# Kernel optimization log

Hardware: AMD Instinct MI355X
Metric: run time of the kernel (lower is better)

The kernel has to match this reference:

```python
import jax, jax.numpy as jnp
import numpy as np

# Stack of L SSA transformer blocks (SMVDR conv_trans stages with sr_ratio=2)
L, B, N, C = 4, 64, 196, 768          # layers, batch(=16 samples x 4 views), tokens, dim
CN = 960                               # c_new = int(C * 1.25)
HID = 3072                             # mlp hidden = 4*C
NH = 12                                # heads
HD, HDK = C // NH, CN // NH            # v head dim 64, q/k head dim 80
SR, HW = 2, 14                         # spatial reduction ratio, sqrt(N)


def _ln(x, g, b, eps):
    m = jnp.mean(x, axis=-1, keepdims=True)
    v = jnp.var(x, axis=-1, keepdims=True)
    return (x - m) * jax.lax.rsqrt(v + eps) * g + b


def setup_inputs() -> dict:
    key = jax.random.key(0)
    ks = jax.random.split(key, 12)
    s = jnp.float32(0.02)

    def rn(k, shape):
        return jax.random.normal(k, shape, jnp.float32) * s

    return {
        "x": jax.random.normal(ks[0], (B, N, C), jnp.float32),
        "q_w": rn(ks[1], (L, C, CN)),                 # q projection (no bias)
        "dw_w": rn(ks[2], (L, C, 1, SR, SR)),         # depthwise reduction conv (OIHW, groups=C)
        "dw_b": jnp.zeros((L, C), jnp.float32),
        "pw_w": rn(ks[3], (L, C, CN)),                # 1x1 conv C -> c_new
        "pw_b": jnp.zeros((L, CN), jnp.float32),
        "lnr_g": jnp.ones((L, CN), jnp.float32),      # norm_act LayerNorm (eps 1e-5)
        "lnr_b": jnp.zeros((L, CN), jnp.float32),
        "k_w": rn(ks[4], (L, CN, CN)),
        "v_w": rn(ks[5], (L, CN, C)),
        "proj_w": rn(ks[6], (L, C, C)),
        "proj_b": jnp.zeros((L, C), jnp.float32),
        "ln1_g": jnp.ones((L, C), jnp.float32),
        "ln1_b": jnp.zeros((L, C), jnp.float32),
        "ln2_g": jnp.ones((L, C), jnp.float32),
        "ln2_b": jnp.zeros((L, C), jnp.float32),
        "fc1_w": rn(ks[7], (L, C, HID)),
        "fc1_b": jnp.zeros((L, HID), jnp.float32),
        "fc2_w": rn(ks[8], (L, HID, C)),
        "fc2_b": jnp.zeros((L, C), jnp.float32),
    }


def reference(x, q_w, dw_w, dw_b, pw_w, pw_b, lnr_g, lnr_b, k_w, v_w,
              proj_w, proj_b, ln1_g, ln1_b, ln2_g, ln2_b,
              fc1_w, fc1_b, fc2_w, fc2_b):
    scale = 1.0 / jnp.sqrt(jnp.float32(HD) * 1.25)   # (head_dim * c_ratio) ** -0.5
    for l in range(L):
        # --- SSA attention branch ---
        y = _ln(x, ln1_g[l], ln1_b[l], 1e-6)
        img = y.transpose(0, 2, 1).reshape(B, C, HW, HW)
        # strided depthwise conv reduction (kernel=stride=sr_ratio, groups=C)
        r = jax.lax.conv_general_dilated(
            img, dw_w[l], window_strides=(SR, SR), padding='VALID',
            feature_group_count=C,
            dimension_numbers=('NCHW', 'OIHW', 'NCHW'))
        r = r + dw_b[l][None, :, None, None]
        r = jnp.einsum('bchw,cd->bhwd', r, pw_w[l]) + pw_b[l]   # 1x1 conv -> (B,7,7,CN)
        r = r.reshape(B, -1, CN)                                 # (B, M=49, CN)
        r = jax.nn.gelu(_ln(r, lnr_g[l], lnr_b[l], 1e-5), approximate=False)
        q = (y @ q_w[l]).reshape(B, N, NH, HDK).transpose(0, 2, 1, 3)   # (B,H,N,80)
        k = (r @ k_w[l]).reshape(B, -1, NH, HDK).transpose(0, 2, 1, 3)  # (B,H,M,80)
        v = (r @ v_w[l]).reshape(B, -1, NH, HD).transpose(0, 2, 1, 3)   # (B,H,M,64)
        attn = jax.nn.softmax(jnp.einsum('bhnd,bhmd->bhnm', q, k) * scale, axis=-1)
        o = jnp.einsum('bhnm,bhmd->bnhd', attn, v).reshape(B, N, C)
        x = x + o @ proj_w[l] + proj_b[l]
        # --- MLP branch ---
        z = _ln(x, ln2_g[l], ln2_b[l], 1e-6)
        h = jax.nn.gelu(z @ fc1_w[l] + fc1_b[l], approximate=False)
        x = x + h @ fc2_w[l] + fc2_b[l]
    return x
```

## Files before the change

### kernel.cpp

```cpp
#include <hip/hip_runtime.h>
#include <hip/hip_bf16.h>
#include <math.h>

#define L_LAYERS 4
#define BSZ 64
#define NTOK 196
#define CDIM 768
#define CNDIM 960
#define HIDDIM 3072
#define NHEAD 12
#define HD 64
#define HDK 80
#define MRED 49
#define ROWS (BSZ*NTOK)
#define RROWS (BSZ*MRED)
#define KVN 1728

typedef __bf16 bf16x8 __attribute__((ext_vector_type(8)));
typedef float f32x4 __attribute__((ext_vector_type(4)));
typedef unsigned short u16x4 __attribute__((ext_vector_type(4)));

static __device__ inline float bf2f(unsigned short u) {
    unsigned int x = ((unsigned int)u) << 16;
    return __builtin_bit_cast(float, x);
}
static __device__ inline unsigned short f2bf(float f) {
    return __builtin_bit_cast(unsigned short, __float2bfloat16(f));
}
static __device__ inline unsigned int pack2bf(float lo, float hi) {
    return (unsigned int)f2bf(lo) | ((unsigned int)f2bf(hi) << 16);
}
static __device__ inline float gelu_f(float x) {
    float t = x * (1.5957691216f + 0.0713548162f * x * x);
    return x * __builtin_amdgcn_rcpf(1.0f + __expf(-t));
}

#define GLLDS16(gsrc, ldst)                                                        \
    __builtin_amdgcn_global_load_lds(                                              \
        (const __attribute__((address_space(1))) unsigned int*)(const void*)(gsrc),\
        (__attribute__((address_space(3))) unsigned int*)(void*)(ldst), 16, 0, 0)

__global__ void transpose_bf16_kernel(const float* __restrict__ src,
                                      unsigned short* __restrict__ dst,
                                      int K, int N, size_t srcLS, size_t dstLS) {
    __shared__ float tile[32][33];
    const float* s = src + (size_t)blockIdx.z * srcLS;
    unsigned short* d = dst + (size_t)blockIdx.z * dstLS;
    int k0 = blockIdx.y * 32, n0 = blockIdx.x * 32;
#pragma unroll
    for (int i = 0; i < 4; i++) {
        int k = k0 + threadIdx.y + i * 8, n = n0 + threadIdx.x;
        if (k < K && n < N) tile[threadIdx.y + i * 8][threadIdx.x] = s[(size_t)k * N + n];
    }
    __syncthreads();
#pragma unroll
    for (int i = 0; i < 4; i++) {
        int n = n0 + threadIdx.y + i * 8, k = k0 + threadIdx.x;
        if (n < N && k < K) d[(size_t)n * K + k] = f2bf(tile[threadIdx.x][threadIdx.y + i * 8]);
    }
}

__global__ void ln_kernel(const float* __restrict__ x, const float* __restrict__ g,
                          const float* __restrict__ b, unsigned short* __restrict__ y,
                          int M, int C, float eps, int do_gelu) {
    int row = blockIdx.x * 4 + (threadIdx.x >> 6);
    int lane = threadIdx.x & 63;
    if (row >= M) return;
    const float* xr = x + (size_t)row * C;
    float s = 0.f, ss = 0.f;
    for (int c = lane; c < C; c += 64) { float v = xr[c]; s += v; ss += v * v; }
#pragma unroll
    for (int off = 32; off; off >>= 1) { s += __shfl_down(s, off); ss += __shfl_down(ss, off); }
    s = __shfl(s, 0); ss = __shfl(ss, 0);
    float mean = s / (float)C;
    float var = ss / (float)C - mean * mean;
    float rstd = rsqrtf(var + eps);
    unsigned short* yr = y + (size_t)row * C;
    for (int c = lane; c < C; c += 64) {
        float v = (xr[c] - mean) * rstd * g[c] + b[c];
        if (do_gelu) v = gelu_f(v);
        yr[c] = f2bf(v);
    }
}

__global__ void dwconv_kernel(const unsigned short* __restrict__ y,
                              const float* __restrict__ w,
                              const float* __restrict__ bias,
                              unsigned short* __restrict__ r0) {
    int bm = blockIdx.x;
    int b = bm / MRED, m = bm % MRED;
    int i = m / 7, j = m % 7;
    int r00 = b * NTOK + (2 * i) * 14 + 2 * j;
    for (int c = threadIdx.x; c < CDIM; c += 256) {
        float acc = bias[c];
        acc += bf2f(y[(size_t)(r00)      * CDIM + c]) * w[c * 4 + 0];
        acc += bf2f(y[(size_t)(r00 + 1)  * CDIM + c]) * w[c * 4 + 1];
        acc += bf2f(y[(size_t)(r00 + 14) * CDIM + c]) * w[c * 4 + 2];
        acc += bf2f(y[(size_t)(r00 + 15) * CDIM + c]) * w[c * 4 + 3];
        r0[(size_t)bm * CDIM + c] = f2bf(acc);
    }
}

template <int MODE, int BN>
__global__ __launch_bounds__(512, 4) void gemm128_kernel(
    const unsigned short* __restrict__ A,
    const unsigned short* __restrict__ Bt,
    const float* __restrict__ bias,
    float* __restrict__ outF,
    unsigned short* __restrict__ outB,
    int M, int N, int K, int NR, int NC) {
    constexpr int NFR = BN / 64;
    constexpr int SLOT = 8192 + BN * 64;
    extern __shared__ __align__(16) char sb[];

    int id = blockIdx.x;
    int gsize = 8 * NC;
    int g = id / gsize;
    int local = id - g * gsize;
    int rbase = g * 8;
    int Gg = NR - rbase; if (Gg > 8) Gg = 8;
    int col = local / Gg;
    int row = rbase + (local - col * Gg);
    int m0 = row * 128, n0 = col * BN;

    int tid = threadIdx.x;
    int w = tid >> 6, lane = tid & 63, quad = lane >> 4, l16 = lane & 15;
    int wm = w >> 2, wn = w & 3;

    int sr = tid >> 2;
    int qs = ((tid & 3) - ((sr >> 1) & 3)) & 3;
    const unsigned short* aS0 = A  + (size_t)(m0 + sr) * K + qs * 8;
    const unsigned short* bS0 = Bt + (size_t)(n0 + sr) * K + qs * 8;
    const unsigned short* bS1 = Bt + (size_t)(n0 + sr + 128) * K + qs * 8;

    int sq16 = ((quad + (l16 >> 1)) & 3) * 16;
    int aOff = (wm * 64 + l16) * 64 + sq16;
    int bOff = 8192 + (wn * (BN / 4) + l16) * 64 + sq16;

    f32x4 zero4 = {0.f, 0.f, 0.f, 0.f};
    f32x4 acc[4][NFR];
#pragma unroll
    for (int mi = 0; mi < 4; mi++)
#pragma unroll
        for (int ni = 0; ni < NFR; ni++) acc[mi][ni] = zero4;

    int NT = K >> 5;

    {
        GLLDS16(aS0, sb + w * 1024);
        GLLDS16(bS0, sb + 8192 + w * 1024);
        if constexpr (BN == 256) GLLDS16(bS1, sb + 16384 + w * 1024);
    }
    asm volatile("s_waitcnt vmcnt(0)" ::: "memory");
    __builtin_amdgcn_s_barrier();

    for (int t = 0; t < NT; ++t) {
        char* sc = sb + (size_t)(t & 1) * SLOT;
        if (t + 1 < NT) {
            char* sp = sb + (size_t)((t + 1) & 1) * SLOT;
            int koff = (t + 1) * 32;
            GLLDS16(aS0 + koff, sp + w * 1024);
            GLLDS16(bS0 + koff, sp + 8192 + w * 1024);
            if constexpr (BN == 256) GLLDS16(bS1 + koff, sp + 16384 + w * 1024);
        }
        bf16x8 af[4], bfr[NFR];
#pragma unroll
        for (int mi = 0; mi < 4; mi++)
            af[mi] = *(const bf16x8*)(sc + aOff + mi * 1024);
#pragma unroll
        for (int ni = 0; ni < NFR; ni++)
            bfr[ni] = *(const bf16x8*)(sc + bOff + ni * 1024);
        __builtin_amdgcn_s_setprio(1);
#pragma unroll
        for (int mi = 0; mi < 4; mi++)
#pragma unroll
            for (int ni = 0; ni < NFR; ni++)
                acc[mi][ni] = __builtin_amdgcn_mfma_f32_16x16x32_bf16(
                    af[mi], bfr[ni], acc[mi][ni], 0, 0, 0);
        __builtin_amdgcn_s_setprio(0);
        asm volatile("s_waitcnt vmcnt(0)" ::: "memory");
        __builtin_amdgcn_s_barrier();
    }

    __syncthreads();
    float* eld = (float*)(sb + w * (BN == 256 ? 4096 : 2048));
    int colbase = n0 + wn * (BN / 4);
#pragma unroll
    for (int mi = 0; mi < 4; mi++) {
#pragma unroll
        for (int ni = 0; ni < NFR; ni++)
#pragma unroll
            for (int rr = 0; rr < 4; rr++)
                eld[(quad * 4 + rr) * (BN / 4) + ni * 16 + l16] = acc[mi][ni][rr];
        int rowb = m0 + wm * 64 + mi * 16;
        constexpr int NP = (BN == 256) ? 4 : 2;
#pragma unroll
        for (int p = 0; p < NP; p++) {
            int r, c;
            if constexpr (BN == 256) { r = p * 4 + quad;        c = l16 * 4; }
            else                     { r = p * 8 + (lane >> 3); c = (lane & 7) * 4; }
            int gr = rowb + r, gc = colbase + c;
            if (gr < M && gc < N) {
                f32x4 v4 = *(f32x4*)(eld + r * (BN / 4) + c);
                if (MODE == 0) {
                    u16x4 h;
#pragma unroll
                    for (int e = 0; e < 4; e++) h[e] = f2bf(v4[e]);
                    *(u16x4*)(outB + (size_t)gr * N + gc) = h;
                } else {
                    f32x4 b4 = *(const f32x4*)(bias + gc);
                    if (MODE == 1) {
                        *(f32x4*)(outF + (size_t)gr * N + gc) = v4 + b4;
                    } else if (MODE == 2) {
                        f32x4 o4 = *(f32x4*)(outF + (size_t)gr * N + gc);
                        *(f32x4*)(outF + (size_t)gr * N + gc) = o4 + v4 + b4;
                    } else {
                        u16x4 h;
#pragma unroll
                        for (int e = 0; e < 4; e++) h[e] = f2bf(gelu_f(v4[e] + b4[e]));
                        *(u16x4*)(outB + (size_t)gr * N + gc) = h;
                    }
                }
            }
        }
    }
}

__global__ __launch_bounds__(512, 4) void attn_kernel(
    const unsigned short* __restrict__ qb,
    const unsigned short* __restrict__ kv,
    unsigned short* __restrict__ ob) {
    __shared__ __align__(16) unsigned short Ks[64 * 96];
    __shared__ __align__(16) unsigned short V2[64 * 136];
    __shared__ __align__(16) unsigned short Os[8 * 16 * 72];

    int bh = blockIdx.x;
    int b = bh / NHEAD, h = bh % NHEAD;
    int tid = threadIdx.x;

    for (int idx = tid; idx < 49 * 8; idx += 512) {
        int m = idx >> 3, c = idx & 7;
        ((unsigned int*)Ks)[m * 48 + 40 + c] = 0u;
    }
    for (int idx = tid; idx < 49 * 10; idx += 512) {
        int m = idx / 10, c = idx % 10;
        bf16x8 v = *(const bf16x8*)(kv + (size_t)(b * MRED + m) * KVN + h * HDK + c * 8);
        *(bf16x8*)(Ks + m * 96 + c * 8) = v;
    }
    for (int idx = tid; idx < 64 * 128; idx += 512) {
        int d = idx >> 7, c = idx & 127;
        int s = c >> 5, q = (c >> 3) & 3, j = c & 7;
        int kt = s * 32 + ((j >> 2) << 4) + q * 4 + (j & 3);
        unsigned short val = 0;
        if (kt < MRED) val = kv[(size_t)(b * MRED + kt) * KVN + 960 + h * HD + d];
        V2[d * 136 + c] = val;
    }
    __syncthreads();

    int wv = tid >> 6, lane = tid & 63, quad = lane >> 4, l16 = lane & 15;
    unsigned short* Ow = Os + wv * 16 * 72;
    const float scale = 0.11180339887498949f;
    f32x4 zero4 = {0.f, 0.f, 0.f, 0.f};

#pragma unroll
    for (int gi = 0; gi < 2; ++gi) {
        int qg = wv + gi * 8;
        if (qg >= 13) break;
        const unsigned short* qrow =
            qb + (size_t)(b * NTOK + qg * 16 + l16) * CNDIM + h * HDK + quad * 8;
        bf16x8 bq0 = *(const bf16x8*)(qrow);
        bf16x8 bq1 = *(const bf16x8*)(qrow + 32);
        bf16x8 bq2 = *(const bf16x8*)(qrow + 64);

        f32x4 sf[4];
#pragma unroll
        for (int kf = 0; kf < 4; kf++) sf[kf] = zero4;
#pragma unroll
        for (int kf = 0; kf < 4; kf++) {
            const unsigned short* kr = Ks + (kf * 16 + l16) * 96 + quad * 8;
            sf[kf] = __builtin_amdgcn_mfma_f32_16x16x32_bf16(
                *(const bf16x8*)(kr), bq0, sf[kf], 0, 0, 0);
            sf[kf] = __builtin_amdgcn_mfma_f32_16x16x32_bf16(
                *(const bf16x8*)(kr + 32), bq1, sf[kf], 0, 0, 0);
            sf[kf] = __builtin_amdgcn_mfma_f32_16x16x32_bf16(
                *(const bf16x8*)(kr + 64), bq2, sf[kf], 0, 0, 0);
        }

        float p[4][4];
        float mx = -1e30f;
#pragma unroll
        for (int kf = 0; kf < 4; kf++)
#pragma unroll
            for (int r = 0; r < 4; r++) {
                float v = sf[kf][r] * scale;
                if (kf == 3) {
                    v = (r == 0 && quad == 0) ? v : -1e30f;
                }
                p[kf][r] = v;
                mx = fmaxf(mx, v);
            }
        mx = fmaxf(mx, __shfl_xor(mx, 16));
        mx = fmaxf(mx, __shfl_xor(mx, 32));
        float sum = 0.f;
#pragma unroll
        for (int kf = 0; kf < 4; kf++)
#pragma unroll
            for (int r = 0; r < 4; r++) {
                float e = __expf(p[kf][r] - mx);
                p[kf][r] = e;
                sum += e;
            }
        sum += __shfl_xor(sum, 16);
        sum += __shfl_xor(sum, 32);
        float inv = 1.0f / sum;
#pragma unroll
        for (int kf = 0; kf < 4; kf++)
#pragma unroll
            for (int r = 0; r < 4; r++) p[kf][r] *= inv;

        unsigned int W[4][2];
#pragma unroll
        for (int kf = 0; kf < 4; kf++) {
            W[kf][0] = pack2bf(p[kf][0], p[kf][1]);
            W[kf][1] = pack2bf(p[kf][2], p[kf][3]);
        }

        f32x4 oacc[4];
#pragma unroll
        for (int df = 0; df < 4; df++) oacc[df] = zero4;
#pragma unroll
        for (int s = 0; s < 2; s++) {
            union { unsigned int u[4]; bf16x8 v; } bb;
            bb.u[0] = W[2 * s][0];
            bb.u[1] = W[2 * s][1];
            bb.u[2] = W[2 * s + 1][0];
            bb.u[3] = W[2 * s + 1][1];
#pragma unroll
            for (int df = 0; df < 4; df++) {
                const unsigned short* vr = V2 + (df * 16 + l16) * 136 + s * 32 + quad * 8;
                oacc[df] = __builtin_amdgcn_mfma_f32_16x16x32_bf16(
                    *(const bf16x8*)(vr), bb.v, oacc[df], 0, 0, 0);
            }
        }

#pragma unroll
        for (int df = 0; df < 4; df++) {
#pragma unroll
            for (int wp = 0; wp < 2; wp++) {
                unsigned int pk = pack2bf(oacc[df][2 * wp], oacc[df][2 * wp + 1]);
                *(unsigned int*)(Ow + l16 * 72 + df * 16 + quad * 4 + 2 * wp) = pk;
            }
        }
        int q = lane >> 2, cch = lane & 3;
        int grow = qg * 16 + q;
        if (grow < NTOK) {
            unsigned short* dst = ob + (size_t)(b * NTOK + grow) * CDIM + h * HD + cch * 8;
            bf16x8 v0 = *(const bf16x8*)(Ow + q * 72 + cch * 8);
            bf16x8 v1 = *(const bf16x8*)(Ow + q * 72 + cch * 8 + 32);
            *(bf16x8*)(dst) = v0;
            *(bf16x8*)(dst + 32) = v1;
        }
    }
}


extern "C" void kernel_launch(void* const* d_in, const int* in_sizes, int n_in,
                              void* d_out, int out_size, void* d_ws, size_t ws_size,
                              hipStream_t stream) {
    (void)in_sizes; (void)n_in; (void)out_size; (void)ws_size;
    const float* x_in   = (const float*)d_in[0];
    const float* q_w    = (const float*)d_in[1];
    const float* dw_w   = (const float*)d_in[2];
    const float* dw_b   = (const float*)d_in[3];
    const float* pw_w   = (const float*)d_in[4];
    const float* pw_b   = (const float*)d_in[5];
    const float* lnr_g  = (const float*)d_in[6];
    const float* lnr_b  = (const float*)d_in[7];
    const float* k_w    = (const float*)d_in[8];
    const float* v_w    = (const float*)d_in[9];
    const float* proj_w = (const float*)d_in[10];
    const float* proj_b = (const float*)d_in[11];
    const float* ln1_g  = (const float*)d_in[12];
    const float* ln1_b  = (const float*)d_in[13];
    const float* ln2_g  = (const float*)d_in[14];
    const float* ln2_b  = (const float*)d_in[15];
    const float* fc1_w  = (const float*)d_in[16];
    const float* fc1_b  = (const float*)d_in[17];
    const float* fc2_w  = (const float*)d_in[18];
    const float* fc2_b  = (const float*)d_in[19];
    float* xout = (float*)d_out;
    char* ws = (char*)d_ws;

    const size_t PL = 8601600;
    const size_t offQ = 0, offPW = 786432, offKV = 1572864,
                 offPJ = 3293184, offF1 = 3883008, offF2 = 6242304;
    unsigned short* W = (unsigned short*)ws;
    char* act = ws + PL * 2 * L_LAYERS;
    unsigned short* y_bf = (unsigned short*)act;
    char* blk = act + (size_t)ROWS * CDIM * 2;
    unsigned short* q_bf  = (unsigned short*)(blk);
    unsigned short* r0_bf = (unsigned short*)(blk + 24084480);
    float*          pw_f  = (float*)        (blk + 29196288);
    unsigned short* r_bf  = (unsigned short*)(blk + 41238528);
    unsigned short* kv_bf = (unsigned short*)(blk + 47628288);
    unsigned short* o_bf  = (unsigned short*)(blk + 58466304);
    unsigned short* h_bf  = (unsigned short*)(blk);
    unsigned short* z_bf  = y_bf;

    hipMemcpyAsync(xout, x_in, (size_t)ROWS * CDIM * sizeof(float),
                   hipMemcpyDeviceToDevice, stream);

    dim3 tb(32, 8);
    transpose_bf16_kernel<<<dim3(CNDIM / 32, CDIM / 32, L_LAYERS), tb, 0, stream>>>(
        q_w, W + offQ, CDIM, CNDIM, (size_t)CDIM * CNDIM, PL);
    transpose_bf16_kernel<<<dim3(CNDIM / 32, CDIM / 32, L_LAYERS), tb, 0, stream>>>(
        pw_w, W + offPW, CDIM, CNDIM, (size_t)CDIM * CNDIM, PL);
    transpose_bf16_kernel<<<dim3(CNDIM / 32, CNDIM / 32, L_LAYERS), tb, 0, stream>>>(
        k_w, W + offKV, CNDIM, CNDIM, (size_t)CNDIM * CNDIM, PL);
    transpose_bf16_kernel<<<dim3(CDIM / 32, CNDIM / 32, L_LAYERS), tb, 0, stream>>>(
        v_w, W + offKV + (size_t)CNDIM * CNDIM, CNDIM, CDIM, (size_t)CNDIM * CDIM, PL);
    transpose_bf16_kernel<<<dim3(CDIM / 32, CDIM / 32, L_LAYERS), tb, 0, stream>>>(
        proj_w, W + offPJ, CDIM, CDIM, (size_t)CDIM * CDIM, PL);
    transpose_bf16_kernel<<<dim3(HIDDIM / 32, CDIM / 32, L_LAYERS), tb, 0, stream>>>(
        fc1_w, W + offF1, CDIM, HIDDIM, (size_t)CDIM * HIDDIM, PL);
    transpose_bf16_kernel<<<dim3(CDIM / 32, HIDDIM / 32, L_LAYERS), tb, 0, stream>>>(
        fc2_w, W + offF2, HIDDIM, CDIM, (size_t)HIDDIM * CDIM, PL);

    for (int l = 0; l < L_LAYERS; l++) {
        const unsigned short* wl = W + (size_t)l * PL;
        ln_kernel<<<ROWS / 4, 256, 0, stream>>>(xout, ln1_g + l * CDIM, ln1_b + l * CDIM,
                                                y_bf, ROWS, CDIM, 1e-6f, 0);
        gemm128_kernel<0, 256><<<98 * 4, 512, 49152, stream>>>(
            y_bf, wl + offQ, nullptr, nullptr, q_bf, ROWS, CNDIM, CDIM, 98, 4);
        dwconv_kernel<<<RROWS, 256, 0, stream>>>(y_bf, dw_w + (size_t)l * CDIM * 4,
                                                 dw_b + l * CDIM, r0_bf);
        gemm128_kernel<1, 128><<<25 * 8, 512, 32768, stream>>>(
            r0_bf, wl + offPW, pw_b + l * CNDIM, pw_f, nullptr, RROWS, CNDIM, CDIM, 25, 8);
        ln_kernel<<<RROWS / 4, 256, 0, stream>>>(pw_f, lnr_g + l * CNDIM, lnr_b + l * CNDIM,
                                                 r_bf, RROWS, CNDIM, 1e-5f, 1);
        gemm128_kernel<0, 128><<<25 * 14, 512, 32768, stream>>>(
            r_bf, wl + offKV, nullptr, nullptr, kv_bf, RROWS, KVN, CNDIM, 25, 14);
        attn_kernel<<<BSZ * NHEAD, 512, 0, stream>>>(q_bf, kv_bf, o_bf);
        gemm128_kernel<2, 256><<<98 * 3, 512, 49152, stream>>>(
            o_bf, wl + offPJ, proj_b + l * CDIM, xout, nullptr, ROWS, CDIM, CDIM, 98, 3);
        ln_kernel<<<ROWS / 4, 256, 0, stream>>>(xout, ln2_g + l * CDIM, ln2_b + l * CDIM,
                                                z_bf, ROWS, CDIM, 1e-6f, 0);
        gemm128_kernel<3, 256><<<98 * 12, 512, 49152, stream>>>(
            z_bf, wl + offF1, fc1_b + l * HIDDIM, nullptr, h_bf, ROWS, HIDDIM, CDIM, 98, 12);
        gemm128_kernel<2, 256><<<98 * 3, 512, 49152, stream>>>(
            h_bf, wl + offF2, fc2_b + l * CDIM, xout, nullptr, ROWS, CDIM, HIDDIM, 98, 3);
    }
}
```

Before: 1.597 ms.

## Triple-buffer GEMM K-loop and split-K residual GEMMs with atomic accumulation

The GEMM main loop moves from a double-buffered LDS pipeline to three slots, keeping two tiles of global-to-LDS loads in flight with partial vmcnt waits. The residual-add GEMMs (proj with split 2, fc2 with split 4) gain a split-K mode: more workgroups each handle a slice of K and add into the output with float atomics, bias added only by the first slice. This targets load latency and the low workgroup count of the N=768 GEMMs (294 blocks). In exchange it needs more LDS per block, which can reduce occupancy, and adds atomic traffic with a nondeterministic summation order.

Result: slower. 4.098 ms (+156.7%).

```diff
diff --git a/kernel.cpp b/kernel.cpp
--- a/kernel.cpp
+++ b/kernel.cpp
@@ -101,7 +101,7 @@
     }
 }
 
-template <int MODE, int BN>
+template <int MODE, int BN, int SK>
 __global__ __launch_bounds__(512, 4) void gemm128_kernel(
     const unsigned short* __restrict__ A,
     const unsigned short* __restrict__ Bt,
@@ -111,9 +111,13 @@
     int M, int N, int K, int NR, int NC) {
     constexpr int NFR = BN / 64;
     constexpr int SLOT = 8192 + BN * 64;
+    constexpr int LPS = (BN == 256) ? 3 : 2;
     extern __shared__ __align__(16) char sb[];
 
     int id = blockIdx.x;
+    int per = NR * NC;
+    int ks = 0;
+    if constexpr (SK > 1) { ks = id / per; id -= ks * per; }
     int gsize = 8 * NC;
     int g = id / gsize;
     int local = id - g * gsize;
@@ -122,6 +126,8 @@
     int col = local / Gg;
     int row = rbase + (local - col * Gg);
     int m0 = row * 128, n0 = col * BN;
+    int KS = K / SK;
+    int k0 = ks * KS;
 
     int tid = threadIdx.x;
     int w = tid >> 6, lane = tid & 63, quad = lane >> 4, l16 = lane & 15;
@@ -129,9 +135,9 @@
 
     int sr = tid >> 2;
     int qs = ((tid & 3) - ((sr >> 1) & 3)) & 3;
-    const unsigned short* aS0 = A  + (size_t)(m0 + sr) * K + qs * 8;
-    const unsigned short* bS0 = Bt + (size_t)(n0 + sr) * K + qs * 8;
-    const unsigned short* bS1 = Bt + (size_t)(n0 + sr + 128) * K + qs * 8;
+    const unsigned short* aS0 = A  + (size_t)(m0 + sr) * K + k0 + qs * 8;
+    const unsigned short* bS0 = Bt + (size_t)(n0 + sr) * K + k0 + qs * 8;
+    const unsigned short* bS1 = Bt + (size_t)(n0 + sr + 128) * K + k0 + qs * 8;
 
     int sq16 = ((quad + (l16 >> 1)) & 3) * 16;
     int aOff = (wm * 64 + l16) * 64 + sq16;
@@ -144,24 +150,32 @@
 #pragma unroll
         for (int ni = 0; ni < NFR; ni++) acc[mi][ni] = zero4;
 
-    int NT = K >> 5;
-
-    {
-        GLLDS16(aS0, sb + w * 1024);
-        GLLDS16(bS0, sb + 8192 + w * 1024);
-        if constexpr (BN == 256) GLLDS16(bS1, sb + 16384 + w * 1024);
-    }
-    asm volatile("s_waitcnt vmcnt(0)" ::: "memory");
+    int NT = KS >> 5;
+
+#define STAGE3(slotptr, tt)                                                \
+    do {                                                                   \
+        int koff_ = (tt) * 32;                                             \
+        GLLDS16(aS0 + koff_, (slotptr) + w * 1024);                        \
+        GLLDS16(bS0 + koff_, (slotptr) + 8192 + w * 1024);                 \
+        if constexpr (BN == 256) GLLDS16(bS1 + koff_, (slotptr) + 16384 + w * 1024); \
+    } while (0)
+
+    STAGE3(sb, 0);
+    if (NT > 1) {
+        STAGE3(sb + SLOT, 1);
+        if constexpr (BN == 256) asm volatile("s_waitcnt vmcnt(3)" ::: "memory");
+        else                     asm volatile("s_waitcnt vmcnt(2)" ::: "memory");
+    } else {
+        asm volatile("s_waitcnt vmcnt(0)" ::: "memory");
+    }
     __builtin_amdgcn_s_barrier();
 
+    int sC = 0;
     for (int t = 0; t < NT; ++t) {
-        char* sc = sb + (size_t)(t & 1) * SLOT;
-        if (t + 1 < NT) {
-            char* sp = sb + (size_t)((t + 1) & 1) * SLOT;
-            int koff = (t + 1) * 32;
-            GLLDS16(aS0 + koff, sp + w * 1024);
-            GLLDS16(bS0 + koff, sp + 8192 + w * 1024);
-            if constexpr (BN == 256) GLLDS16(bS1 + koff, sp + 16384 + w * 1024);
+        char* sc = sb + (size_t)sC * SLOT;
+        if (t + 2 < NT) {
+            int sP = sC + 2; if (sP >= 3) sP -= 3;
+            STAGE3(sb + (size_t)sP * SLOT, t + 2);
         }
         bf16x8 af[4], bfr[NFR];
 #pragma unroll
@@ -178,9 +192,16 @@
                 acc[mi][ni] = __builtin_amdgcn_mfma_f32_16x16x32_bf16(
                     af[mi], bfr[ni], acc[mi][ni], 0, 0, 0);
         __builtin_amdgcn_s_setprio(0);
-        asm volatile("s_waitcnt vmcnt(0)" ::: "memory");
+        if (t + 2 < NT) {
+            if constexpr (BN == 256) asm volatile("s_waitcnt vmcnt(3)" ::: "memory");
+            else                     asm volatile("s_waitcnt vmcnt(2)" ::: "memory");
+        } else {
+            asm volatile("s_waitcnt vmcnt(0)" ::: "memory");
+        }
         __builtin_amdgcn_s_barrier();
-    }
+        sC++; if (sC == 3) sC = 0;
+    }
+#undef STAGE3
 
     __syncthreads();
     float* eld = (float*)(sb + w * (BN == 256 ? 4096 : 2048));
@@ -212,8 +233,18 @@
                     if (MODE == 1) {
                         *(f32x4*)(outF + (size_t)gr * N + gc) = v4 + b4;
                     } else if (MODE == 2) {
-                        f32x4 o4 = *(f32x4*)(outF + (size_t)gr * N + gc);
-                        *(f32x4*)(outF + (size_t)gr * N + gc) = o4 + v4 + b4;
+                        if constexpr (SK == 1) {
+                            f32x4 o4 = *(f32x4*)(outF + (size_t)gr * N + gc);
+                            *(f32x4*)(outF + (size_t)gr * N + gc) = o4 + v4 + b4;
+                        } else {
+                            f32x4 v = v4;
+                            if (ks == 0) v = v + b4;
+                            float* dp = outF + (size_t)gr * N + gc;
+                            atomicAdd(dp + 0, v[0]);
+                            atomicAdd(dp + 1, v[1]);
+                            atomicAdd(dp + 2, v[2]);
+                            atomicAdd(dp + 3, v[3]);
+                        }
                     } else {
                         u16x4 h;
 #pragma unroll
@@ -391,6 +422,19 @@
     float* xout = (float*)d_out;
     char* ws = (char*)d_ws;
 
+    static bool attr_done = false;
+    if (!attr_done) {
+        hipFuncSetAttribute(reinterpret_cast<const void*>(&gemm128_kernel<0, 256, 1>),
+                            hipFuncAttributeMaxDynamicSharedMemorySize, 73728);
+        hipFuncSetAttribute(reinterpret_cast<const void*>(&gemm128_kernel<2, 256, 2>),
+                            hipFuncAttributeMaxDynamicSharedMemorySize, 73728);
+        hipFuncSetAttribute(reinterpret_cast<const void*>(&gemm128_kernel<2, 256, 4>),
+                            hipFuncAttributeMaxDynamicSharedMemorySize, 73728);
+        hipFuncSetAttribute(reinterpret_cast<const void*>(&gemm128_kernel<3, 256, 1>),
+                            hipFuncAttributeMaxDynamicSharedMemorySize, 73728);
+        attr_done = true;
+    }
+
     const size_t PL = 8601600;
     const size_t offQ = 0, offPW = 786432, offKV = 1572864,
                  offPJ = 3293184, offF1 = 3883008, offF2 = 6242304;
@@ -430,24 +474,24 @@
         const unsigned short* wl = W + (size_t)l * PL;
         ln_kernel<<<ROWS / 4, 256, 0, stream>>>(xout, ln1_g + l * CDIM, ln1_b + l * CDIM,
                                                 y_bf, ROWS, CDIM, 1e-6f, 0);
-        gemm128_kernel<0, 256><<<98 * 4, 512, 49152, stream>>>(
+        gemm128_kernel<0, 256, 1><<<98 * 4, 512, 73728, stream>>>(
             y_bf, wl + offQ, nullptr, nullptr, q_bf, ROWS, CNDIM, CDIM, 98, 4);
         dwconv_kernel<<<RROWS, 256, 0, stream>>>(y_bf, dw_w + (size_t)l * CDIM * 4,
                                                  dw_b + l * CDIM, r0_bf);
-        gemm128_kernel<1, 128><<<25 * 8, 512, 32768, stream>>>(
+        gemm128_kernel<1, 128, 1><<<25 * 8, 512, 49152, stream>>>(
             r0_bf, wl + offPW, pw_b + l * CNDIM, pw_f, nullptr, RROWS, CNDIM, CDIM, 25, 8);
         ln_kernel<<<RROWS / 4, 256, 0, stream>>>(pw_f, lnr_g + l * CNDIM, lnr_b + l * CNDIM,
                                                  r_bf, RROWS, CNDIM, 1e-5f, 1);
-        gemm128_kernel<0, 128><<<25 * 14, 512, 32768, stream>>>(
+        gemm128_kernel<0, 128, 1><<<25 * 14, 512, 49152, stream>>>(
             r_bf, wl + offKV, nullptr, nullptr, kv_bf, RROWS, KVN, CNDIM, 25, 14);
         attn_kernel<<<BSZ * NHEAD, 512, 0, stream>>>(q_bf, kv_bf, o_bf);
-        gemm128_kernel<2, 256><<<98 * 3, 512, 49152, stream>>>(
+        gemm128_kernel<2, 256, 2><<<98 * 3 * 2, 512, 73728, stream>>>(
             o_bf, wl + offPJ, proj_b + l * CDIM, xout, nullptr, ROWS, CDIM, CDIM, 98, 3);
         ln_kernel<<<ROWS / 4, 256, 0, stream>>>(xout, ln2_g + l * CDIM, ln2_b + l * CDIM,
                                                 z_bf, ROWS, CDIM, 1e-6f, 0);
-        gemm128_kernel<3, 256><<<98 * 12, 512, 49152, stream>>>(
+        gemm128_kernel<3, 256, 1><<<98 * 12, 512, 73728, stream>>>(
             z_bf, wl + offF1, fc1_b + l * HIDDIM, nullptr, h_bf, ROWS, HIDDIM, CDIM, 98, 12);
-        gemm128_kernel<2, 256><<<98 * 3, 512, 49152, stream>>>(
+        gemm128_kernel<2, 256, 4><<<98 * 3 * 4, 512, 73728, stream>>>(
             h_bf, wl + offF2, fc2_b + l * CDIM, xout, nullptr, ROWS, CDIM, HIDDIM, 98, 3);
     }
 }
```

## Switch GEMM to 128x128 tiles with 64-deep K stages and XOR swizzle

Applied to the files above, without the earlier changes.

The bf16 GEMM kernel drops its BN=256 variant and always uses 128x128 output tiles. Each pipeline stage now covers 64 elements of K instead of 32, staged into a 64KB double-buffered LDS layout with an XOR-swizzled address pattern, and two MFMA sub-steps run per stage. The aim is to halve the number of barriers and waits per K and to give the large GEMMs more blocks. In exchange, each block reuses less data per tile, LDS use per block grows (which can lower occupancy), and the dynamic shared memory attribute has to be raised.

After: 1.549 ms. -3.0%, faster.

```diff
diff --git a/kernel.cpp b/kernel.cpp
--- a/kernel.cpp
+++ b/kernel.cpp
@@ -101,7 +101,7 @@
     }
 }
 
-template <int MODE, int BN>
+template <int MODE>
 __global__ __launch_bounds__(512, 4) void gemm128_kernel(
     const unsigned short* __restrict__ A,
     const unsigned short* __restrict__ Bt,
@@ -109,8 +109,6 @@
     float* __restrict__ outF,
     unsigned short* __restrict__ outB,
     int M, int N, int K, int NR, int NC) {
-    constexpr int NFR = BN / 64;
-    constexpr int SLOT = 8192 + BN * 64;
     extern __shared__ __align__(16) char sb[];
 
     int id = blockIdx.x;
@@ -121,87 +119,105 @@
     int Gg = NR - rbase; if (Gg > 8) Gg = 8;
     int col = local / Gg;
     int row = rbase + (local - col * Gg);
-    int m0 = row * 128, n0 = col * BN;
+    int m0 = row * 128, n0 = col * 128;
 
     int tid = threadIdx.x;
     int w = tid >> 6, lane = tid & 63, quad = lane >> 4, l16 = lane & 15;
     int wm = w >> 2, wn = w & 3;
 
-    int sr = tid >> 2;
-    int qs = ((tid & 3) - ((sr >> 1) & 3)) & 3;
-    const unsigned short* aS0 = A  + (size_t)(m0 + sr) * K + qs * 8;
-    const unsigned short* bS0 = Bt + (size_t)(n0 + sr) * K + qs * 8;
-    const unsigned short* bS1 = Bt + (size_t)(n0 + sr + 128) * K + qs * 8;
-
-    int sq16 = ((quad + (l16 >> 1)) & 3) * 16;
-    int aOff = (wm * 64 + l16) * 64 + sq16;
-    int bOff = 8192 + (wn * (BN / 4) + l16) * 64 + sq16;
+    int r = tid >> 3;
+    int qc = (tid & 7) ^ (r & 7);
+    const unsigned short* aS0 = A  + (size_t)(m0 + r) * K + qc * 8;
+    const unsigned short* aS1 = A  + (size_t)(m0 + r + 64) * K + qc * 8;
+    const unsigned short* bS0 = Bt + (size_t)(n0 + r) * K + qc * 8;
+    const unsigned short* bS1 = Bt + (size_t)(n0 + r + 64) * K + qc * 8;
+
+    int s7 = l16 & 7;
+    int sq0 = ((0 + quad) ^ s7) * 16;
+    int sq1 = ((4 + quad) ^ s7) * 16;
+    int aBase = (wm * 64 + l16) * 128;
+    int bBase = 16384 + (wn * 32 + l16) * 128;
 
     f32x4 zero4 = {0.f, 0.f, 0.f, 0.f};
-    f32x4 acc[4][NFR];
+    f32x4 acc[4][2];
 #pragma unroll
     for (int mi = 0; mi < 4; mi++)
 #pragma unroll
-        for (int ni = 0; ni < NFR; ni++) acc[mi][ni] = zero4;
-
-    int NT = K >> 5;
-
-    {
-        GLLDS16(aS0, sb + w * 1024);
-        GLLDS16(bS0, sb + 8192 + w * 1024);
-        if constexpr (BN == 256) GLLDS16(bS1, sb + 16384 + w * 1024);
-    }
+        for (int ni = 0; ni < 2; ni++) acc[mi][ni] = zero4;
+
+    int NT = K >> 6;
+
+#define STAGE64(slotptr, tt)                                     \
+    do {                                                         \
+        int ko_ = (tt) * 64;                                     \
+        GLLDS16(aS0 + ko_, (slotptr) + w * 1024);                \
+        GLLDS16(aS1 + ko_, (slotptr) + 8192  + w * 1024);        \
+        GLLDS16(bS0 + ko_, (slotptr) + 16384 + w * 1024);        \
+        GLLDS16(bS1 + ko_, (slotptr) + 24576 + w * 1024);        \
+    } while (0)
+
+    STAGE64(sb, 0);
     asm volatile("s_waitcnt vmcnt(0)" ::: "memory");
     __builtin_amdgcn_s_barrier();
 
     for (int t = 0; t < NT; ++t) {
-        char* sc = sb + (size_t)(t & 1) * SLOT;
+        char* sc = sb + (size_t)(t & 1) * 32768;
         if (t + 1 < NT) {
-            char* sp = sb + (size_t)((t + 1) & 1) * SLOT;
-            int koff = (t + 1) * 32;
-            GLLDS16(aS0 + koff, sp + w * 1024);
-            GLLDS16(bS0 + koff, sp + 8192 + w * 1024);
-            if constexpr (BN == 256) GLLDS16(bS1 + koff, sp + 16384 + w * 1024);
-        }
-        bf16x8 af[4], bfr[NFR];
+            char* sp = sb + (size_t)((t + 1) & 1) * 32768;
+            STAGE64(sp, t + 1);
+        }
+        bf16x8 af[4], bfr[2];
 #pragma unroll
         for (int mi = 0; mi < 4; mi++)
-            af[mi] = *(const bf16x8*)(sc + aOff + mi * 1024);
-#pragma unroll
-        for (int ni = 0; ni < NFR; ni++)
-            bfr[ni] = *(const bf16x8*)(sc + bOff + ni * 1024);
+            af[mi] = *(const bf16x8*)(sc + aBase + mi * 2048 + sq0);
+#pragma unroll
+        for (int ni = 0; ni < 2; ni++)
+            bfr[ni] = *(const bf16x8*)(sc + bBase + ni * 2048 + sq0);
         __builtin_amdgcn_s_setprio(1);
 #pragma unroll
         for (int mi = 0; mi < 4; mi++)
 #pragma unroll
-            for (int ni = 0; ni < NFR; ni++)
+            for (int ni = 0; ni < 2; ni++)
+                acc[mi][ni] = __builtin_amdgcn_mfma_f32_16x16x32_bf16(
+                    af[mi], bfr[ni], acc[mi][ni], 0, 0, 0);
+        __builtin_amdgcn_s_setprio(0);
+#pragma unroll
+        for (int mi = 0; mi < 4; mi++)
+            af[mi] = *(const bf16x8*)(sc + aBase + mi * 2048 + sq1);
+#pragma unroll
+        for (int ni = 0; ni < 2; ni++)
+            bfr[ni] = *(const bf16x8*)(sc + bBase + ni * 2048 + sq1);
+        __builtin_amdgcn_s_setprio(1);
+#pragma unroll
+        for (int mi = 0; mi < 4; mi++)
+#pragma unroll
+            for (int ni = 0; ni < 2; ni++)
                 acc[mi][ni] = __builtin_amdgcn_mfma_f32_16x16x32_bf16(
                     af[mi], bfr[ni], acc[mi][ni], 0, 0, 0);
         __builtin_amdgcn_s_setprio(0);
         asm volatile("s_waitcnt vmcnt(0)" ::: "memory");
         __builtin_amdgcn_s_barrier();
     }
+#undef STAGE64
 
     __syncthreads();
-    float* eld = (float*)(sb + w * (BN == 256 ? 4096 : 2048));
-    int colbase = n0 + wn * (BN / 4);
+    float* eld = (float*)(sb + w * 2048);
+    int colbase = n0 + wn * 32;
 #pragma unroll
     for (int mi = 0; mi < 4; mi++) {
 #pragma unroll
-        for (int ni = 0; ni < NFR; ni++)
+        for (int ni = 0; ni < 2; ni++)
 #pragma unroll
             for (int rr = 0; rr < 4; rr++)
-                eld[(quad * 4 + rr) * (BN / 4) + ni * 16 + l16] = acc[mi][ni][rr];
+                eld[(quad * 4 + rr) * 32 + ni * 16 + l16] = acc[mi][ni][rr];
         int rowb = m0 + wm * 64 + mi * 16;
-        constexpr int NP = (BN == 256) ? 4 : 2;
-#pragma unroll
-        for (int p = 0; p < NP; p++) {
-            int r, c;
-            if constexpr (BN == 256) { r = p * 4 + quad;        c = l16 * 4; }
-            else                     { r = p * 8 + (lane >> 3); c = (lane & 7) * 4; }
-            int gr = rowb + r, gc = colbase + c;
+#pragma unroll
+        for (int p = 0; p < 2; p++) {
+            int r2 = p * 8 + (lane >> 3);
+            int c2 = (lane & 7) * 4;
+            int gr = rowb + r2, gc = colbase + c2;
             if (gr < M && gc < N) {
-                f32x4 v4 = *(f32x4*)(eld + r * (BN / 4) + c);
+                f32x4 v4 = *(f32x4*)(eld + r2 * 32 + c2);
                 if (MODE == 0) {
                     u16x4 h;
 #pragma unroll
@@ -391,6 +407,19 @@
     float* xout = (float*)d_out;
     char* ws = (char*)d_ws;
 
+    static bool attr_done = false;
+    if (!attr_done) {
+        hipFuncSetAttribute(reinterpret_cast<const void*>(&gemm128_kernel<0>),
+                            hipFuncAttributeMaxDynamicSharedMemorySize, 65536);
+        hipFuncSetAttribute(reinterpret_cast<const void*>(&gemm128_kernel<1>),
+                            hipFuncAttributeMaxDynamicSharedMemorySize, 65536);
+        hipFuncSetAttribute(reinterpret_cast<const void*>(&gemm128_kernel<2>),
+                            hipFuncAttributeMaxDynamicSharedMemorySize, 65536);
+        hipFuncSetAttribute(reinterpret_cast<const void*>(&gemm128_kernel<3>),
+                            hipFuncAttributeMaxDynamicSharedMemorySize, 65536);
+        attr_done = true;
+    }
+
     const size_t PL = 8601600;
     const size_t offQ = 0, offPW = 786432, offKV = 1572864,
                  offPJ = 3293184, offF1 = 3883008, offF2 = 6242304;
@@ -430,24 +459,24 @@
         const unsigned short* wl = W + (size_t)l * PL;
         ln_kernel<<<ROWS / 4, 256, 0, stream>>>(xout, ln1_g + l * CDIM, ln1_b + l * CDIM,
                                                 y_bf, ROWS, CDIM, 1e-6f, 0);
-        gemm128_kernel<0, 256><<<98 * 4, 512, 49152, stream>>>(
-            y_bf, wl + offQ, nullptr, nullptr, q_bf, ROWS, CNDIM, CDIM, 98, 4);
+        gemm128_kernel<0><<<98 * 8, 512, 65536, stream>>>(
+            y_bf, wl + offQ, nullptr, nullptr, q_bf, ROWS, CNDIM, CDIM, 98, 8);
         dwconv_kernel<<<RROWS, 256, 0, stream>>>(y_bf, dw_w + (size_t)l * CDIM * 4,
                                                  dw_b + l * CDIM, r0_bf);
-        gemm128_kernel<1, 128><<<25 * 8, 512, 32768, stream>>>(
+        gemm128_kernel<1><<<25 * 8, 512, 65536, stream>>>(
             r0_bf, wl + offPW, pw_b + l * CNDIM, pw_f, nullptr, RROWS, CNDIM, CDIM, 25, 8);
         ln_kernel<<<RROWS / 4, 256, 0, stream>>>(pw_f, lnr_g + l * CNDIM, lnr_b + l * CNDIM,
                                                  r_bf, RROWS, CNDIM, 1e-5f, 1);
-        gemm128_kernel<0, 128><<<25 * 14, 512, 32768, stream>>>(
+        gemm128_kernel<0><<<25 * 14, 512, 65536, stream>>>(
             r_bf, wl + offKV, nullptr, nullptr, kv_bf, RROWS, KVN, CNDIM, 25, 14);
         attn_kernel<<<BSZ * NHEAD, 512, 0, stream>>>(q_bf, kv_bf, o_bf);
-        gemm128_kernel<2, 256><<<98 * 3, 512, 49152, stream>>>(
-            o_bf, wl + offPJ, proj_b + l * CDIM, xout, nullptr, ROWS, CDIM, CDIM, 98, 3);
+        gemm128_kernel<2><<<98 * 6, 512, 65536, stream>>>(
+            o_bf, wl + offPJ, proj_b + l * CDIM, xout, nullptr, ROWS, CDIM, CDIM, 98, 6);
         ln_kernel<<<ROWS / 4, 256, 0, stream>>>(xout, ln2_g + l * CDIM, ln2_b + l * CDIM,
                                                 z_bf, ROWS, CDIM, 1e-6f, 0);
-        gemm128_kernel<3, 256><<<98 * 12, 512, 49152, stream>>>(
-            z_bf, wl + offF1, fc1_b + l * HIDDIM, nullptr, h_bf, ROWS, HIDDIM, CDIM, 98, 12);
-        gemm128_kernel<2, 256><<<98 * 3, 512, 49152, stream>>>(
-            h_bf, wl + offF2, fc2_b + l * CDIM, xout, nullptr, ROWS, CDIM, HIDDIM, 98, 3);
-    }
-}
+        gemm128_kernel<3><<<98 * 24, 512, 65536, stream>>>(
+            z_bf, wl + offF1, fc1_b + l * HIDDIM, nullptr, h_bf, ROWS, HIDDIM, CDIM, 98, 24);
+        gemm128_kernel<2><<<98 * 6, 512, 65536, stream>>>(
+            h_bf, wl + offF2, fc2_b + l * CDIM, xout, nullptr, ROWS, CDIM, HIDDIM, 98, 6);
+    }
+}
```
